# Optimization experiments

Measured on AMD Instinct MI355X. Metric: run time of the kernel, lower is better.

Reference implementation:

```python
import jax, jax.numpy as jnp
import numpy as np

DIM = 1024
HEADS = 8
DIM_HEAD = 64
INNER = HEADS * DIM_HEAD  # 512


def setup_inputs() -> dict:
    key = jax.random.key(0)
    k1, k2, k3, k4 = jax.random.split(key, 4)
    x = jax.random.normal(k1, (4, 4096, DIM), dtype=jnp.float32)
    # torch nn.Linear weights: [out_features, in_features]
    w_qkv = jax.random.normal(k2, (INNER * 3, DIM), dtype=jnp.float32) * (DIM ** -0.5)
    w_out = jax.random.normal(k3, (DIM, INNER), dtype=jnp.float32) * (INNER ** -0.5)
    b_out = jax.random.normal(k4, (DIM,), dtype=jnp.float32) * 0.01
    return {"x": x, "w_qkv": w_qkv, "w_out": w_out, "b_out": b_out}


def reference(x, w_qkv, w_out, b_out):
    b, n, _ = x.shape
    h, dh = HEADS, DIM_HEAD
    qkv = x @ w_qkv.T  # [b, n, 3*inner]
    q, k, v = jnp.split(qkv, 3, axis=-1)
    # [b, n, inner] -> [b, h, n, dh]
    reshape = lambda t: t.reshape(b, n, h, dh).transpose(0, 2, 1, 3)
    q, k, v = reshape(q), reshape(k), reshape(v)
    k = jax.nn.softmax(k, axis=-1)
    context = jnp.einsum('bhnd,bhne->bhde', k, v)   # [b, h, dh, dh]
    out = jnp.einsum('bhnd,bhde->bhne', q, context)  # [b, h, n, dh]
    out = out.transpose(0, 2, 1, 3).reshape(b, n, h * dh)
    return out @ w_out.T + b_out
```

## Files before the change

### kernel.cpp

```cpp
#include <hip/hip_runtime.h>
#include <hip/hip_bf16.h>

using bf16 = __hip_bfloat16;
typedef __attribute__((ext_vector_type(8))) short short8;
typedef __attribute__((ext_vector_type(4))) float floatx4;

#define NB 4
#define NSEQ 4096
#define DIM 1024
#define INNER 512
#define TOK (NB * NSEQ)


__device__ inline unsigned short f2bf(float x) {
  union { bf16 h; unsigned short u; } c; c.h = __float2bfloat16(x); return c.u;
}
__device__ inline float bf2f(unsigned short u) {
  return __uint_as_float((unsigned)u << 16);
}
__device__ inline void cvt8(const float* __restrict__ src, bf16* dst) {
  const float4 a = ((const float4*)src)[0];
  const float4 b = ((const float4*)src)[1];
  union { uint4 u; bf16 h[8]; } p;
  p.h[0] = __float2bfloat16(a.x); p.h[1] = __float2bfloat16(a.y);
  p.h[2] = __float2bfloat16(a.z); p.h[3] = __float2bfloat16(a.w);
  p.h[4] = __float2bfloat16(b.x); p.h[5] = __float2bfloat16(b.y);
  p.h[6] = __float2bfloat16(b.z); p.h[7] = __float2bfloat16(b.w);
  *(uint4*)dst = p.u;
}

__device__ inline void gload_lds16(const bf16* g, bf16* ldsbase) {
  __builtin_amdgcn_global_load_lds(
      (const __attribute__((address_space(1))) void*)g,
      (__attribute__((address_space(3))) void*)ldsbase, 16, 0, 0);
}

__global__ __launch_bounds__(256)
void convert_x(const float* __restrict__ x, bf16* __restrict__ xb) {
  const size_t i = (size_t)blockIdx.x * 256 + threadIdx.x;
  cvt8(x + i * 8, xb + i * 8);
}

__global__ __launch_bounds__(256)
void copy16(const uint4* __restrict__ src, uint4* __restrict__ dst) {
  const size_t i = (size_t)blockIdx.x * 256 + threadIdx.x;
  dst[i] = src[i];
}

__global__ void zero_ctx(float* __restrict__ ctx) {
  ((float4*)ctx)[blockIdx.x * 256 + threadIdx.x] = make_float4(0.f, 0.f, 0.f, 0.f);
}

template <typename TO, bool BIAS>
__global__ __launch_bounds__(256, 4)
void gemm_bt(const bf16* __restrict__ A, int lda,
             const bf16* __restrict__ W, size_t wbatch, int mTiles,
             const float* __restrict__ bias,
             TO* __restrict__ C, int ldc, int K) {
  __shared__ __align__(16) bf16 As[128 * 64];
  __shared__ __align__(16) bf16 Bs[128 * 64];

  const int tid    = threadIdx.x;
  const int p      = blockIdx.x;
  const int m_tile = p % mTiles;
  const int n_tile = p / mTiles;
  const int m0     = m_tile * 128;
  const int n0     = n_tile * 128;
  if (wbatch) W += (size_t)(m_tile >> 5) * wbatch;

  const int wave = tid >> 6;
  const int lane = tid & 63;
  const int wr   = (wave >> 1) * 64;
  const int wc   = (wave & 1) * 64;
  const int quad = lane >> 4;
  const int r16  = lane & 15;
  const int rxor = r16 & 7;
  const int lrow = lane >> 3;
  const int lcol = lane & 7;
  const int gchunk = lcol ^ lrow;

  floatx4 acc[4][4];
#pragma unroll
  for (int i = 0; i < 4; ++i)
#pragma unroll
    for (int j = 0; j < 4; ++j) acc[i][j] = (floatx4)0.0f;

  const int ksteps = K >> 6;
  for (int kt = 0; kt < ksteps; ++kt) {
    const int k0 = kt << 6;
#pragma unroll
    for (int t = 0; t < 4; ++t) {
      const int s   = wave * 4 + t;
      const int row = s * 8 + lrow;
      gload_lds16(A + (size_t)(m0 + row) * lda + k0 + gchunk * 8, As + s * 512);
      gload_lds16(W + (size_t)(n0 + row) * K   + k0 + gchunk * 8, Bs + s * 512);
    }
    __syncthreads();
#pragma unroll
    for (int kk = 0; kk < 64; kk += 32) {
      const int cbase = kk >> 3;
      short8 af[4], bfg[4];
#pragma unroll
      for (int i = 0; i < 4; ++i)
        af[i] = *(const short8*)(As + (wr + i * 16 + r16) * 64 + (((quad + cbase) ^ rxor) << 3));
#pragma unroll
      for (int j = 0; j < 4; ++j)
        bfg[j] = *(const short8*)(Bs + (wc + j * 16 + r16) * 64 + (((quad + cbase) ^ rxor) << 3));
#pragma unroll
      for (int i = 0; i < 4; ++i)
#pragma unroll
        for (int j = 0; j < 4; ++j)
          acc[i][j] = __builtin_amdgcn_mfma_f32_16x16x32_bf16(af[i], bfg[j], acc[i][j], 0, 0, 0);
    }
    __syncthreads();
  }

#pragma unroll
  for (int j = 0; j < 4; ++j) {
    const int col = n0 + wc + j * 16 + r16;
    const float bv = BIAS ? bias[col] : 0.0f;
#pragma unroll
    for (int i = 0; i < 4; ++i) {
      const int rowb = m0 + wr + i * 16 + quad * 4;
#pragma unroll
      for (int r = 0; r < 4; ++r) {
        const float v = acc[i][j][r] + bv;
        if constexpr (sizeof(TO) == 2)
          C[(size_t)(rowb + r) * ldc + col] = __float2bfloat16(v);
        else
          C[(size_t)(rowb + r) * ldc + col] = v;
      }
    }
  }
}

__global__ __launch_bounds__(256)
void softmax_context(const unsigned short* __restrict__ kv, float* __restrict__ ctx) {
  __shared__ unsigned short skT[64 * 130];
  __shared__ unsigned short vT [64 * 130];

  const int tid   = threadIdx.x;
  const int wave  = tid >> 6;
  const int lane  = tid & 63;
  const int bh    = blockIdx.x >> 4;
  const int slice = blockIdx.x & 15;
  const int b     = bh >> 3, h = bh & 7;

  const int quad = lane >> 4;
  const int r16  = lane & 15;
  const int d0   = wave * 16;

  floatx4 acc[4];
#pragma unroll
  for (int j = 0; j < 4; ++j) acc[j] = (floatx4)0.0f;

  const int rgrp = tid >> 3;
  const int c    = tid & 7;

  for (int ch = 0; ch < 2; ++ch) {
#pragma unroll
    for (int p = 0; p < 4; ++p) {
      const int r = p * 32 + rgrp;
      const size_t rowbase =
          (size_t)(b * NSEQ + slice * 256 + ch * 128 + r) * 1024 + h * 64;
      const uint4 k8 = *(const uint4*)(kv + rowbase + c * 8);
      const uint4 v8 = *(const uint4*)(kv + rowbase + 512 + c * 8);
      const unsigned short* kb = (const unsigned short*)&k8;
      const unsigned short* vb = (const unsigned short*)&v8;

      float kf[8];
#pragma unroll
      for (int j = 0; j < 8; ++j) kf[j] = bf2f(kb[j]);
      float mx = kf[0];
#pragma unroll
      for (int j = 1; j < 8; ++j) mx = fmaxf(mx, kf[j]);
      mx = fmaxf(mx, __shfl_xor(mx, 1, 64));
      mx = fmaxf(mx, __shfl_xor(mx, 2, 64));
      mx = fmaxf(mx, __shfl_xor(mx, 4, 64));
      float e[8]; float s = 0.0f;
#pragma unroll
      for (int j = 0; j < 8; ++j) { e[j] = __expf(kf[j] - mx); s += e[j]; }
      s += __shfl_xor(s, 1, 64);
      s += __shfl_xor(s, 2, 64);
      s += __shfl_xor(s, 4, 64);
      const float inv = 1.0f / s;
#pragma unroll
      for (int j = 0; j < 8; ++j) {
        const int d = c * 8 + j;
        skT[d * 130 + r] = f2bf(e[j] * inv);
        vT [d * 130 + r] = vb[j];
      }
    }
    __syncthreads();

#pragma unroll
    for (int kk = 0; kk < 4; ++kk) {
      const int kof = kk * 32 + quad * 8;
      union { short8 v; unsigned u[4]; } afr;
      {
        const unsigned* q = (const unsigned*)(skT + (d0 + r16) * 130 + kof);
        afr.u[0] = q[0]; afr.u[1] = q[1]; afr.u[2] = q[2]; afr.u[3] = q[3];
      }
#pragma unroll
      for (int j = 0; j < 4; ++j) {
        union { short8 v; unsigned u[4]; } bfr;
        const unsigned* q = (const unsigned*)(vT + (j * 16 + r16) * 130 + kof);
        bfr.u[0] = q[0]; bfr.u[1] = q[1]; bfr.u[2] = q[2]; bfr.u[3] = q[3];
        acc[j] = __builtin_amdgcn_mfma_f32_16x16x32_bf16(afr.v, bfr.v, acc[j], 0, 0, 0);
      }
    }
    __syncthreads();
  }

  float* cg = ctx + (size_t)bh * 4096;
#pragma unroll
  for (int j = 0; j < 4; ++j) {
    const int e = j * 16 + r16;
#pragma unroll
    for (int r = 0; r < 4; ++r) {
      const int d = d0 + quad * 4 + r;
      atomicAdd(cg + d * 64 + e, acc[j][r]);
    }
  }
}

__global__ __launch_bounds__(256)
void transpose_wq(const float* __restrict__ wq, bf16* __restrict__ wqT) {
  __shared__ unsigned short t[64 * 68];
  const int tid = threadIdx.x;
  const int c0  = blockIdx.x * 64;
  const int r0  = blockIdx.y * 64;

#pragma unroll
  for (int l = 0; l < 4; ++l) {
    const int s = l * 256 + tid;
    const int row = s >> 4, col4 = s & 15;
    const float4 v = *(const float4*)(wq + (size_t)(r0 + row) * 1024 + c0 + col4 * 4);
    t[row * 68 + col4 * 4 + 0] = f2bf(v.x);
    t[row * 68 + col4 * 4 + 1] = f2bf(v.y);
    t[row * 68 + col4 * 4 + 2] = f2bf(v.z);
    t[row * 68 + col4 * 4 + 3] = f2bf(v.w);
  }
  __syncthreads();
#pragma unroll
  for (int l = 0; l < 2; ++l) {
    const int s = l * 256 + tid;
    const int cc = s >> 3, g = s & 7;
    union { uint4 u; unsigned short h[8]; } o;
#pragma unroll
    for (int u = 0; u < 8; ++u) o.h[u] = t[(g * 8 + u) * 68 + cc];
    *(uint4*)((unsigned short*)wqT + (size_t)(c0 + cc) * 512 + r0 + g * 8) = o.u;
  }
}

__global__ __launch_bounds__(256)
void build_m2(const float* __restrict__ w_out, const float* __restrict__ ctx,
              bf16* __restrict__ M2) {
  __shared__ unsigned short wo_s[128 * 68];
  __shared__ __align__(16) float ctx_s[4096];

  const int tid = threadIdx.x;
  const int bh  = blockIdx.y;
  const int b   = bh >> 3, h = bh & 7;
  const int o0  = blockIdx.x * 128;

#pragma unroll
  for (int l = 0; l < 8; ++l) {
    const int s = l * 256 + tid;
    const int row = s >> 4, col4 = s & 15;
    const float4 v = *(const float4*)(w_out + (size_t)(o0 + row) * 512 + h * 64 + col4 * 4);
    wo_s[row * 68 + col4 * 4 + 0] = f2bf(v.x);
    wo_s[row * 68 + col4 * 4 + 1] = f2bf(v.y);
    wo_s[row * 68 + col4 * 4 + 2] = f2bf(v.z);
    wo_s[row * 68 + col4 * 4 + 3] = f2bf(v.w);
  }
  const float4* cg = (const float4*)(ctx + (size_t)bh * 4096);
#pragma unroll
  for (int l = 0; l < 4; ++l) ((float4*)ctx_s)[l * 256 + tid] = cg[l * 256 + tid];
  __syncthreads();

  const int o_loc = tid & 127;
  const int dbase = (tid >> 7) * 32;
  float acc[32];
#pragma unroll
  for (int d = 0; d < 32; ++d) acc[d] = 0.0f;

  for (int e = 0; e < 64; ++e) {
    const float wf = bf2f(wo_s[o_loc * 68 + e]);
#pragma unroll
    for (int d = 0; d < 32; ++d)
      acc[d] += wf * ctx_s[(dbase + d) * 64 + e];
  }

  union { uint4 u[4]; unsigned short h[32]; } o;
#pragma unroll
  for (int d = 0; d < 32; ++d) o.h[d] = f2bf(acc[d]);
  unsigned short* dst = (unsigned short*)M2 + (size_t)(b * 1024 + o0 + o_loc) * 512 + h * 64 + dbase;
#pragma unroll
  for (int i = 0; i < 4; ++i) ((uint4*)dst)[i] = o.u[i];
}

extern "C" void kernel_launch(void* const* d_in, const int* in_sizes, int n_in,
                              void* d_out, int out_size, void* d_ws, size_t ws_size,
                              hipStream_t stream) {
  const float* x     = (const float*)d_in[0];
  const float* w_qkv = (const float*)d_in[1];
  const float* w_out = (const float*)d_in[2];
  const float* b_out = (const float*)d_in[3];
  float* out = (float*)d_out;

  char* xbuf = (char*)d_in[0];
  char* wbuf = (char*)d_in[1];

  bf16*  wkvb = (bf16*)xbuf;
  bf16*  M2   = (bf16*)(xbuf + (size_t)2097152);
  bf16*  W2   = (bf16*)(xbuf + (size_t)6291456);
  bf16*  xb   = (bf16*)(xbuf + (size_t)33554432);
  bf16*  xbhi_stage = (bf16*)d_out;
  bf16*  kv   = (bf16*)d_out;
  bf16*  wqT  = (bf16*)(wbuf + 2097152);
  float* ctx  = (float*)(wbuf + 3145728);

  convert_x<<<4096, 256, 0, stream>>>(x + (size_t)8192 * DIM, xbhi_stage);
  convert_x<<<4096, 256, 0, stream>>>(x, xb);
  copy16<<<4096, 256, 0, stream>>>((const uint4*)xbhi_stage,
                                   (uint4*)(xb + (size_t)8192 * DIM));
  convert_x<<<512, 256, 0, stream>>>(w_qkv + (size_t)INNER * DIM, wkvb);

  gemm_bt<bf16, false><<<1024, 256, 0, stream>>>(
      xb, DIM, wkvb, 0, 128, nullptr, kv, 1024, DIM);

  zero_ctx<<<128, 256, 0, stream>>>(ctx);
  transpose_wq<<<dim3(16, 8), 256, 0, stream>>>(w_qkv, wqT);

  softmax_context<<<512, 256, 0, stream>>>((const unsigned short*)kv, ctx);

  build_m2<<<dim3(8, 32), 256, 0, stream>>>(w_out, ctx, M2);

  gemm_bt<bf16, false><<<256, 256, 0, stream>>>(
      M2, 512, wqT, 0, 32, nullptr, W2, 1024, 512);

  gemm_bt<float, true><<<1024, 256, 0, stream>>>(
      xb, DIM, W2, (size_t)1048576, 128, b_out, out, DIM, DIM);
}
```

Measured before the change: 255.7 us.

## Add 256x256-tile 8-wave GEMM with ping-pong LDS pipeline for big GEMMs

Adds a new GEMM kernel using 256x256 output tiles, 512 threads, double-buffered LDS staged by direct global-to-LDS loads with XOR swizzling, and interleaved fragment loads and MFMA quadrants under barriers and priority hints. It replaces the 128-tile GEMM for the KV projection and the final output projection. The larger tile raises arithmetic intensity and overlaps the next tile's loads with compute. In exchange it uses much more LDS and registers, and launches only 256 blocks, which may underfill the GPU.

```diff
diff --git a/kernel.cpp b/kernel.cpp
--- a/kernel.cpp
+++ b/kernel.cpp
@@ -34,6 +34,8 @@
       (const __attribute__((address_space(1))) void*)g,
       (__attribute__((address_space(3))) void*)ldsbase, 16, 0, 0);
 }
+
+#define WAITVM(N) asm volatile("s_waitcnt vmcnt(" #N ")" ::: "memory")
 
 __global__ __launch_bounds__(256)
 void convert_x(const float* __restrict__ x, bf16* __restrict__ xb) {
@@ -134,6 +136,152 @@
   }
 }
 
+template <typename TO, bool BIAS>
+__global__ __launch_bounds__(512, 2)
+void gemm256(const bf16* __restrict__ A, int lda,
+             const bf16* __restrict__ W, size_t wbatch, int mTiles,
+             const float* __restrict__ bias,
+             TO* __restrict__ C, int ldc, int K) {
+  __shared__ __align__(16) bf16 As[2 * 16384];
+  __shared__ __align__(16) bf16 Bs[2 * 16384];
+
+  const int tid    = threadIdx.x;
+  const int p      = blockIdx.x;
+  const int m_tile = p % mTiles;
+  const int n_tile = p / mTiles;
+  const int m0     = m_tile * 256;
+  const int n0     = n_tile * 256;
+  if (wbatch) W += (size_t)(m_tile >> 4) * wbatch;
+
+  const int wave = tid >> 6;
+  const int lane = tid & 63;
+  const int wm   = wave >> 2;
+  const int wn   = wave & 3;
+  const int quad = lane >> 4;
+  const int r16  = lane & 15;
+  const int rxor = r16 & 7;
+  const int lrow = lane >> 3;
+  const int lcol = lane & 7;
+  const int gchunk = lcol ^ lrow;
+
+  const int nk = K >> 6;
+
+  auto stageA = [&](int T) {
+    bf16* lp = As + (T & 1) * 16384;
+#pragma unroll
+    for (int c = 0; c < 4; ++c) {
+      const int rb = c * 64 + wave * 8;
+      gload_lds16(A + (size_t)(m0 + rb + lrow) * lda + T * 64 + gchunk * 8,
+                  lp + rb * 64);
+    }
+  };
+  auto stageB = [&](int T) {
+    bf16* lp = Bs + (T & 1) * 16384;
+#pragma unroll
+    for (int c = 0; c < 4; ++c) {
+      const int rb = c * 64 + wave * 8;
+      gload_lds16(W + (size_t)(n0 + rb + lrow) * K + T * 64 + gchunk * 8,
+                  lp + rb * 64);
+    }
+  };
+
+  floatx4 acc[8][4];
+#pragma unroll
+  for (int i = 0; i < 8; ++i)
+#pragma unroll
+    for (int j = 0; j < 4; ++j) acc[i][j] = (floatx4)0.0f;
+
+  short8 a[4][2], b[2][2];
+
+#define LDA_FRAGS(mh) do {                                                    \
+  _Pragma("unroll")                                                           \
+  for (int i = 0; i < 4; ++i) {                                               \
+    const bf16* base = As + db * 16384 +                                      \
+        (wm * 128 + (mh) * 64 + i * 16 + r16) * 64;                           \
+    a[i][0] = *(const short8*)(base + ((quad ^ rxor) << 3));                  \
+    a[i][1] = *(const short8*)(base + (((4 + quad) ^ rxor) << 3));            \
+  } } while (0)
+
+#define LDB_FRAGS(nh) do {                                                    \
+  _Pragma("unroll")                                                           \
+  for (int j = 0; j < 2; ++j) {                                               \
+    const bf16* base = Bs + db * 16384 +                                      \
+        (wn * 64 + (nh) * 32 + j * 16 + r16) * 64;                            \
+    b[j][0] = *(const short8*)(base + ((quad ^ rxor) << 3));                  \
+    b[j][1] = *(const short8*)(base + (((4 + quad) ^ rxor) << 3));            \
+  } } while (0)
+
+#define MFMA_QUAD(mh, nh) do {                                                \
+  _Pragma("unroll")                                                           \
+  for (int i = 0; i < 4; ++i)                                                 \
+  _Pragma("unroll")                                                           \
+  for (int j = 0; j < 2; ++j) {                                               \
+    acc[(mh)*4+i][(nh)*2+j] = __builtin_amdgcn_mfma_f32_16x16x32_bf16(        \
+        a[i][0], b[j][0], acc[(mh)*4+i][(nh)*2+j], 0, 0, 0);                  \
+    acc[(mh)*4+i][(nh)*2+j] = __builtin_amdgcn_mfma_f32_16x16x32_bf16(        \
+        a[i][1], b[j][1], acc[(mh)*4+i][(nh)*2+j], 0, 0, 0);                  \
+  } } while (0)
+
+  stageA(0); stageB(0);
+  if (nk > 1) { stageA(1); WAITVM(4); }
+  else        { WAITVM(0); }
+  __builtin_amdgcn_s_barrier();
+
+  for (int T = 0; T < nk; ++T) {
+    const int db = T & 1;
+    LDA_FRAGS(0); LDB_FRAGS(0);
+    if (T + 1 < nk) stageB(T + 1);
+    __builtin_amdgcn_s_barrier();
+    __builtin_amdgcn_s_setprio(1);
+    MFMA_QUAD(0, 0);
+    __builtin_amdgcn_s_setprio(0);
+    __builtin_amdgcn_s_barrier();
+    LDB_FRAGS(1);
+    __builtin_amdgcn_s_barrier();
+    __builtin_amdgcn_s_setprio(1);
+    MFMA_QUAD(0, 1);
+    __builtin_amdgcn_s_setprio(0);
+    __builtin_amdgcn_s_barrier();
+    LDA_FRAGS(1);
+    __builtin_amdgcn_s_barrier();
+    __builtin_amdgcn_s_setprio(1);
+    MFMA_QUAD(1, 1);
+    __builtin_amdgcn_s_setprio(0);
+    __builtin_amdgcn_s_barrier();
+    LDB_FRAGS(0);
+    if (T + 2 < nk) stageA(T + 2);
+    __builtin_amdgcn_s_barrier();
+    __builtin_amdgcn_s_setprio(1);
+    MFMA_QUAD(1, 0);
+    __builtin_amdgcn_s_setprio(0);
+    if (T < nk - 2) WAITVM(4);
+    else            WAITVM(0);
+    __builtin_amdgcn_s_barrier();
+  }
+
+#undef LDA_FRAGS
+#undef LDB_FRAGS
+#undef MFMA_QUAD
+
+#pragma unroll
+  for (int jj = 0; jj < 4; ++jj) {
+    const int col = n0 + wn * 64 + jj * 16 + r16;
+    const float bv = BIAS ? bias[col] : 0.0f;
+#pragma unroll
+    for (int ii = 0; ii < 8; ++ii) {
+      const int rowb = m0 + wm * 128 + ii * 16 + quad * 4;
+#pragma unroll
+      for (int r = 0; r < 4; ++r) {
+        const float v = acc[ii][jj][r] + bv;
+        if constexpr (sizeof(TO) == 2)
+          C[(size_t)(rowb + r) * ldc + col] = __float2bfloat16(v);
+        else
+          C[(size_t)(rowb + r) * ldc + col] = v;
+      }
+    }
+  }
+}
+
 __global__ __launch_bounds__(256)
 void softmax_context(const unsigned short* __restrict__ kv, float* __restrict__ ctx) {
   __shared__ unsigned short skT[64 * 130];
@@ -327,8 +475,8 @@
                                    (uint4*)(xb + (size_t)8192 * DIM));
   convert_x<<<512, 256, 0, stream>>>(w_qkv + (size_t)INNER * DIM, wkvb);
 
-  gemm_bt<bf16, false><<<1024, 256, 0, stream>>>(
-      xb, DIM, wkvb, 0, 128, nullptr, kv, 1024, DIM);
+  gemm256<bf16, false><<<256, 512, 0, stream>>>(
+      xb, DIM, wkvb, 0, 64, nullptr, kv, 1024, DIM);
 
   zero_ctx<<<128, 256, 0, stream>>>(ctx);
   transpose_wq<<<dim3(16, 8), 256, 0, stream>>>(w_qkv, wqT);
@@ -340,6 +488,6 @@
   gemm_bt<bf16, false><<<256, 256, 0, stream>>>(
       M2, 512, wqT, 0, 32, nullptr, W2, 1024, 512);
 
-  gemm_bt<float, true><<<1024, 256, 0, stream>>>(
-      xb, DIM, W2, (size_t)1048576, 128, b_out, out, DIM, DIM);
-}
+  gemm256<float, true><<<256, 512, 0, stream>>>(
+      xb, DIM, W2, (size_t)1048576, 64, b_out, out, DIM, DIM);
+}
```

After: 256.7 us. Within noise of the previous version (+0.4%).
